# Kernel tuning notes

Measured on AMD Instinct MI355X. Metric: run time of the kernel, lower is better.

Reference implementation:

```python
import jax, jax.numpy as jnp
import numpy as np

MAX_ITER = 3  # module default init kwarg
B, S = 16, 128


def setup_inputs() -> dict:
    key = jax.random.key(0)
    k1, k2, k3 = jax.random.split(key, 3)
    s_span = jax.random.normal(k1, (B, S, S), dtype=jnp.float32)
    s_pair = jax.random.normal(k2, (B, S, S, S), dtype=jnp.float32)
    mask = jax.random.randint(k3, (B, S, S), 0, 2).astype(jnp.bool_)
    return {"s_span": s_span, "s_pair": s_pair, "mask": mask}


def reference(s_span, s_pair, mask):
    # Faithful batch-first translation of MFVIConstituency.mfvi + sigmoid.
    # torch code works in [S, S, B] layout; here we keep [B, S, S].
    seq_len = mask.shape[1]
    idx = jnp.arange(seq_len)
    # ls[i,j]=min(i,j), rs[i,j]=max(i,j) (stack(where(ones)).sort(0) trick)
    ls = jnp.minimum(idx[:, None], idx[None, :])  # [S, S]
    rs = jnp.maximum(idx[:, None], idx[None, :])  # [S, S]
    # exclude k == min(i,j) and k == max(i,j): [S, S, S] over (i, j, k)
    ne = (ls[:, :, None] != idx[None, None, :]) & (rs[:, :, None] != idx[None, None, :])
    # span_mask broadcast in torch aligns trailing dims -> indexed at (j, k):
    # mask2o[b,i,j,k] &= mask[b,k,j] | mask[b,j,k]
    span = mask | jnp.swapaxes(mask, 1, 2)  # [B, S, S] symmetric
    # mask2o[b,i,j,k] = mask[b,i,j] & ne[i,j,k] & span[b,j,k]
    mask2o = mask[:, :, :, None] & ne[None, :, :, :] & span[:, None, :, :]
    sp = s_pair * mask2o.astype(s_pair.dtype)  # [B, S, S, S]
    q = s_span
    for _ in range(MAX_ITER):
        q = jax.nn.sigmoid(q)
        # q_new[b,i,j] = s_span[b,i,j] + sum_k q[b,i,k] * sp[b,i,j,k]
        q = s_span + jnp.einsum('bik,bijk->bij', q, sp)
    return jax.nn.sigmoid(q)  # marginals [B, S, S]
```

## Files before the change

kernel.cpp:

```cpp
#include <hip/hip_runtime.h>
#include <hip/hip_bf16.h>


#define S 128
#define MB_STRIDE 132
#define PART_STRIDE 33

static __device__ __forceinline__ float fsig(float x) {
    return __builtin_amdgcn_rcpf(1.0f + __expf(-x));
}

__global__ __launch_bounds__(256, 2) void pack_masks(
    const int* __restrict__ mask, unsigned* __restrict__ spanw,
    unsigned* __restrict__ miw)
{
    __shared__ unsigned char mb[S * MB_STRIDE];
    const int t = threadIdx.x, b = blockIdx.x;
    const int* mrow = mask + (long long)b * (S * S);
    #pragma unroll
    for (int s2 = 0; s2 < 16; ++s2) {
        int f4 = t + 256 * s2;
        int j  = f4 >> 5;
        int k0 = (f4 & 31) * 4;
        int4 v = *(const int4*)(mrow + f4 * 4);
        unsigned packed = (v.x ? 1u : 0u)
                        | ((v.y ? 1u : 0u) << 8)
                        | ((v.z ? 1u : 0u) << 16)
                        | ((v.w ? 1u : 0u) << 24);
        *(unsigned*)(mb + j * MB_STRIDE + k0) = packed;
    }
    __syncthreads();
    #pragma unroll
    for (int r = 0; r < 2; ++r) {
        int task = t * 2 + r;
        int j = task >> 2, w = task & 3;
        unsigned sbits = 0, mbits = 0;
        #pragma unroll
        for (int c = 0; c < 32; ++c) {
            int k = w * 32 + c;
            unsigned mjk = mb[j * MB_STRIDE + k];
            unsigned mkj = mb[k * MB_STRIDE + j];
            sbits |= ((mjk | mkj) ? 1u : 0u) << c;
            mbits |= (mjk ? 1u : 0u) << c;
        }
        spanw[(b * S + j) * 4 + w] = sbits;
        miw  [(b * S + j) * 4 + w] = mbits;
    }
}

__global__ __launch_bounds__(256, 4) void mfvi_main(
    const float* __restrict__ s_span,
    const float* __restrict__ s_pair,
    const unsigned* __restrict__ spanw,
    const unsigned* __restrict__ miw,
    float* __restrict__ out)
{
    __shared__ float         part[S * PART_STRIDE];
    __shared__ unsigned      sw_l[S * 4];
    __shared__ float         prow[S];
    __shared__ float         qsv [S];
    __shared__ unsigned char act [S];
    __shared__ int           nact_s;

    const int t  = threadIdx.x;
    const int bi = blockIdx.x;
    const int i  = bi & (S - 1);
    const int b  = bi >> 7;
    const int row0 = t >> 5;
    const int c4   = (t & 31) * 4;
    const float* tile = s_pair + (long long)bi * (S * S);

    if (t < S) *(uint4*)&sw_l[t * 4] = *(const uint4*)&spanw[(b * S + t) * 4];
    if (t < S) {
        float sv = s_span[(long long)bi * S + t];
        qsv[t]  = sv;
        prow[t] = fsig(sv);
    }
    if (t < 64) {
        unsigned w0 = miw[(b * S + i) * 4 + (t >> 5)];
        bool a0 = (w0 >> (t & 31)) & 1u;
        unsigned long long b0 = __ballot(a0);
        int p0 = __popcll(b0 & ((1ull << t) - 1ull));
        if (a0) act[p0] = (unsigned char)t;
        int n0 = __popcll(b0);
        int j1 = t + 64;
        unsigned w1 = miw[(b * S + i) * 4 + (j1 >> 5)];
        bool a1 = (w1 >> (j1 & 31)) & 1u;
        unsigned long long b1 = __ballot(a1);
        int p1 = n0 + __popcll(b1 & ((1ull << t) - 1ull));
        if (a1) act[p1] = (unsigned char)j1;
        if (t == 0) nact_s = n0 + __popcll(b1);
    }
    __syncthreads();
    const int nact = nact_s;

    if (t < S) {
        bool mine = (miw[(b * S + i) * 4 + (t >> 5)] >> (t & 31)) & 1u;
        if (!mine) out[(long long)bi * S + t] = prow[t];
    }

    float4 v[16];
    #pragma unroll
    for (int s = 0; s < 16; ++s) {
        int idx = row0 + 8 * s;
        if (idx < nact) {
            int j = act[idx];
            v[s] = *(const float4*)(tile + j * S + c4);
        } else {
            v[s] = make_float4(0.f, 0.f, 0.f, 0.f);
        }
    }

    #pragma unroll
    for (int s = 0; s < 16; ++s) {
        int idx = row0 + 8 * s;
        if (idx < nact) {
            int j = act[idx];
            unsigned cw = sw_l[j * 4 + (c4 >> 5)];
            int lo = i < j ? i : j, hi = i < j ? j : i;
            if ((lo >> 5) == (c4 >> 5)) cw &= ~(1u << (lo & 31));
            if ((hi >> 5) == (c4 >> 5)) cw &= ~(1u << (hi & 31));
            unsigned cs = cw >> (c4 & 31);
            int m0 = ((int)(cs << 31)) >> 31;
            int m1 = ((int)(cs << 30)) >> 31;
            int m2 = ((int)(cs << 29)) >> 31;
            int m3 = ((int)(cs << 28)) >> 31;
            v[s].x = __int_as_float(__float_as_int(v[s].x) & m0);
            v[s].y = __int_as_float(__float_as_int(v[s].y) & m1);
            v[s].z = __int_as_float(__float_as_int(v[s].z) & m2);
            v[s].w = __int_as_float(__float_as_int(v[s].w) & m3);
        }
    }

    const int pcol = t & 31;
    #pragma unroll
    for (int it = 0; it < 3; ++it) {
        float4 p = *(const float4*)&prow[c4];
        #pragma unroll
        for (int s = 0; s < 16; ++s) {
            int idx = row0 + 8 * s;
            if (idx < nact) {
                float acc = v[s].x * p.x + v[s].y * p.y + v[s].z * p.z + v[s].w * p.w;
                part[idx * PART_STRIDE + pcol] = acc;
            }
        }
        __syncthreads();
        if (t < nact) {
            int j = act[t];
            float sum = 0.f;
            #pragma unroll
            for (int c = 0; c < 32; ++c) sum += part[t * PART_STRIDE + c];
            float q = qsv[j] + sum;
            if (it < 2) prow[j] = fsig(q);
            else        out[(long long)bi * S + j] = fsig(q);
        }
        if (it < 2) __syncthreads();
    }
}

extern "C" void kernel_launch(void* const* d_in, const int* in_sizes, int n_in,
                              void* d_out, int out_size, void* d_ws, size_t ws_size,
                              hipStream_t stream) {
    const float* s_span = (const float*)d_in[0];
    const float* s_pair = (const float*)d_in[1];
    const int*   mask   = (const int*)d_in[2];
    float*       out    = (float*)d_out;

    int num_rows = in_sizes[0] / S;
    int B        = in_sizes[2] / (S * S);

    unsigned* ws_span = (unsigned*)d_ws;
    unsigned* ws_mi   = ws_span + (size_t)B * S * 4;

    pack_masks<<<B, 256, 0, stream>>>(mask, ws_span, ws_mi);
    mfvi_main<<<num_rows, 256, 0, stream>>>(s_span, s_pair, ws_span, ws_mi, out);
}
```

Measured before the change: 191.2 us.

## Reduce row dot-products with wave shuffles and precompute active-row lists in pack kernel

The LDS partial-sum buffer and its extra barrier per iteration are replaced by an in-register butterfly reduction using xor shuffles across 32 lanes, and prow is double-buffered so only one barrier per iteration remains. Compaction of active rows moves from the main kernel into the mask-packing kernel, which writes per-row index lists and counts to workspace. Span masking is folded into the tile load loop, and unmasked outputs are written straight from the raw mask. The main kernel's startup gets simpler and LDS use drops, at the cost of more shuffle instructions, more predicated single-lane sigmoid work, and extra workspace traffic in the pack kernel.

```diff
diff --git a/kernel.cpp b/kernel.cpp
--- a/kernel.cpp
+++ b/kernel.cpp
@@ -4,15 +4,16 @@
 
 #define S 128
 #define MB_STRIDE 132
-#define PART_STRIDE 33
 
 static __device__ __forceinline__ float fsig(float x) {
     return __builtin_amdgcn_rcpf(1.0f + __expf(-x));
 }
 
 __global__ __launch_bounds__(256, 2) void pack_masks(
-    const int* __restrict__ mask, unsigned* __restrict__ spanw,
-    unsigned* __restrict__ miw)
+    const int* __restrict__ mask,
+    unsigned* __restrict__ spanw,
+    unsigned char* __restrict__ actg,
+    int* __restrict__ nactg)
 {
     __shared__ unsigned char mb[S * MB_STRIDE];
     const int t = threadIdx.x, b = blockIdx.x;
@@ -30,37 +31,50 @@
         *(unsigned*)(mb + j * MB_STRIDE + k0) = packed;
     }
     __syncthreads();
+
     #pragma unroll
     for (int r = 0; r < 2; ++r) {
         int task = t * 2 + r;
         int j = task >> 2, w = task & 3;
-        unsigned sbits = 0, mbits = 0;
+        unsigned sbits = 0;
         #pragma unroll
         for (int c = 0; c < 32; ++c) {
             int k = w * 32 + c;
-            unsigned mjk = mb[j * MB_STRIDE + k];
-            unsigned mkj = mb[k * MB_STRIDE + j];
-            sbits |= ((mjk | mkj) ? 1u : 0u) << c;
-            mbits |= (mjk ? 1u : 0u) << c;
+            sbits |= ((mb[j * MB_STRIDE + k] | mb[k * MB_STRIDE + j]) ? 1u : 0u) << c;
         }
         spanw[(b * S + j) * 4 + w] = sbits;
-        miw  [(b * S + j) * 4 + w] = mbits;
+    }
+
+    {
+        int wave = t >> 6, lane = t & 63;
+        for (int r = 0; r < 32; ++r) {
+            int i = wave * 32 + r;
+            unsigned char* dst = actg + (long long)(b * S + i) * S;
+            bool a0 = mb[i * MB_STRIDE + lane] != 0;
+            unsigned long long b0 = __ballot(a0);
+            int n0 = __popcll(b0);
+            if (a0) dst[__popcll(b0 & ((1ull << lane) - 1ull))] = (unsigned char)lane;
+            bool a1 = mb[i * MB_STRIDE + 64 + lane] != 0;
+            unsigned long long b1 = __ballot(a1);
+            if (a1) dst[n0 + __popcll(b1 & ((1ull << lane) - 1ull))] = (unsigned char)(64 + lane);
+            if (lane == 0) nactg[b * S + i] = n0 + __popcll(b1);
+        }
     }
 }
 
 __global__ __launch_bounds__(256, 4) void mfvi_main(
     const float* __restrict__ s_span,
     const float* __restrict__ s_pair,
+    const int* __restrict__ mask,
     const unsigned* __restrict__ spanw,
-    const unsigned* __restrict__ miw,
+    const unsigned char* __restrict__ actg,
+    const int* __restrict__ nactg,
     float* __restrict__ out)
 {
-    __shared__ float         part[S * PART_STRIDE];
     __shared__ unsigned      sw_l[S * 4];
-    __shared__ float         prow[S];
+    __shared__ float         prow2[2][S];
     __shared__ float         qsv [S];
-    __shared__ unsigned char act [S];
-    __shared__ int           nact_s;
+    __shared__ unsigned char act_l[S];
 
     const int t  = threadIdx.x;
     const int bi = blockIdx.x;
@@ -69,90 +83,75 @@
     const int row0 = t >> 5;
     const int c4   = (t & 31) * 4;
     const float* tile = s_pair + (long long)bi * (S * S);
+    const int nact = nactg[bi];
 
-    if (t < S) *(uint4*)&sw_l[t * 4] = *(const uint4*)&spanw[(b * S + t) * 4];
     if (t < S) {
+        act_l[t] = actg[(long long)bi * S + t];
+        *(uint4*)&sw_l[t * 4] = *(const uint4*)&spanw[(b * S + t) * 4];
         float sv = s_span[(long long)bi * S + t];
-        qsv[t]  = sv;
-        prow[t] = fsig(sv);
-    }
-    if (t < 64) {
-        unsigned w0 = miw[(b * S + i) * 4 + (t >> 5)];
-        bool a0 = (w0 >> (t & 31)) & 1u;
-        unsigned long long b0 = __ballot(a0);
-        int p0 = __popcll(b0 & ((1ull << t) - 1ull));
-        if (a0) act[p0] = (unsigned char)t;
-        int n0 = __popcll(b0);
-        int j1 = t + 64;
-        unsigned w1 = miw[(b * S + i) * 4 + (j1 >> 5)];
-        bool a1 = (w1 >> (j1 & 31)) & 1u;
-        unsigned long long b1 = __ballot(a1);
-        int p1 = n0 + __popcll(b1 & ((1ull << t) - 1ull));
-        if (a1) act[p1] = (unsigned char)j1;
-        if (t == 0) nact_s = n0 + __popcll(b1);
+        qsv[t] = sv;
+        float p0 = fsig(sv);
+        prow2[0][t] = p0;
+        prow2[1][t] = p0;
+        if (!mask[(long long)bi * S + t])
+            out[(long long)bi * S + t] = p0;
     }
     __syncthreads();
-    const int nact = nact_s;
-
-    if (t < S) {
-        bool mine = (miw[(b * S + i) * 4 + (t >> 5)] >> (t & 31)) & 1u;
-        if (!mine) out[(long long)bi * S + t] = prow[t];
-    }
 
     float4 v[16];
     #pragma unroll
     for (int s = 0; s < 16; ++s) {
         int idx = row0 + 8 * s;
         if (idx < nact) {
-            int j = act[idx];
-            v[s] = *(const float4*)(tile + j * S + c4);
+            int j = act_l[idx];
+            float4 x = *(const float4*)(tile + j * S + c4);
+            unsigned cw = sw_l[j * 4 + (c4 >> 5)];
+            int lo = i < j ? i : j, hi = i < j ? j : i;
+            if ((lo >> 5) == (c4 >> 5)) cw &= ~(1u << (lo & 31));
+            if ((hi >> 5) == (c4 >> 5)) cw &= ~(1u << (hi & 31));
+            unsigned cs = cw >> (c4 & 31);
+            x.x = __int_as_float(__float_as_int(x.x) & (((int)(cs << 31)) >> 31));
+            x.y = __int_as_float(__float_as_int(x.y) & (((int)(cs << 30)) >> 31));
+            x.z = __int_as_float(__float_as_int(x.z) & (((int)(cs << 29)) >> 31));
+            x.w = __int_as_float(__float_as_int(x.w) & (((int)(cs << 28)) >> 31));
+            v[s] = x;
         } else {
             v[s] = make_float4(0.f, 0.f, 0.f, 0.f);
         }
     }
 
     #pragma unroll
-    for (int s = 0; s < 16; ++s) {
-        int idx = row0 + 8 * s;
-        if (idx < nact) {
-            int j = act[idx];
-            unsigned cw = sw_l[j * 4 + (c4 >> 5)];
-            int lo = i < j ? i : j, hi = i < j ? j : i;
-            if ((lo >> 5) == (c4 >> 5)) cw &= ~(1u << (lo & 31));
-            if ((hi >> 5) == (c4 >> 5)) cw &= ~(1u << (hi & 31));
-            unsigned cs = cw >> (c4 & 31);
-            int m0 = ((int)(cs << 31)) >> 31;
-            int m1 = ((int)(cs << 30)) >> 31;
-            int m2 = ((int)(cs << 29)) >> 31;
-            int m3 = ((int)(cs << 28)) >> 31;
-            v[s].x = __int_as_float(__float_as_int(v[s].x) & m0);
-            v[s].y = __int_as_float(__float_as_int(v[s].y) & m1);
-            v[s].z = __int_as_float(__float_as_int(v[s].z) & m2);
-            v[s].w = __int_as_float(__float_as_int(v[s].w) & m3);
-        }
-    }
-
-    const int pcol = t & 31;
-    #pragma unroll
     for (int it = 0; it < 3; ++it) {
-        float4 p = *(const float4*)&prow[c4];
+        const float* pr = prow2[it & 1];
+        float*       pw = prow2[(it + 1) & 1];
+        float4 p = *(const float4*)&pr[c4];
+        float acc[16];
         #pragma unroll
         for (int s = 0; s < 16; ++s) {
             int idx = row0 + 8 * s;
-            if (idx < nact) {
-                float acc = v[s].x * p.x + v[s].y * p.y + v[s].z * p.z + v[s].w * p.w;
-                part[idx * PART_STRIDE + pcol] = acc;
+            acc[s] = (idx < nact)
+                   ? (v[s].x * p.x + v[s].y * p.y + v[s].z * p.z + v[s].w * p.w)
+                   : 0.f;
+        }
+        #pragma unroll
+        for (int s = 0; s < 16; ++s) {
+            acc[s] += __shfl_xor(acc[s], 1);
+            acc[s] += __shfl_xor(acc[s], 2);
+            acc[s] += __shfl_xor(acc[s], 4);
+            acc[s] += __shfl_xor(acc[s], 8);
+            acc[s] += __shfl_xor(acc[s], 16);
+        }
+        if ((t & 31) == 0) {
+            #pragma unroll
+            for (int s = 0; s < 16; ++s) {
+                int idx = row0 + 8 * s;
+                if (idx < nact) {
+                    int j = act_l[idx];
+                    float q = qsv[j] + acc[s];
+                    if (it < 2) pw[j] = fsig(q);
+                    else        out[(long long)bi * S + j] = fsig(q);
+                }
             }
-        }
-        __syncthreads();
-        if (t < nact) {
-            int j = act[t];
-            float sum = 0.f;
-            #pragma unroll
-            for (int c = 0; c < 32; ++c) sum += part[t * PART_STRIDE + c];
-            float q = qsv[j] + sum;
-            if (it < 2) prow[j] = fsig(q);
-            else        out[(long long)bi * S + j] = fsig(q);
         }
         if (it < 2) __syncthreads();
     }
@@ -169,9 +168,11 @@
     int num_rows = in_sizes[0] / S;
     int B        = in_sizes[2] / (S * S);
 
-    unsigned* ws_span = (unsigned*)d_ws;
-    unsigned* ws_mi   = ws_span + (size_t)B * S * 4;
+    unsigned*      ws_span = (unsigned*)d_ws;
+    unsigned char* ws_act  = (unsigned char*)(ws_span + (size_t)B * S * 4);
+    int*           ws_nact = (int*)(ws_act + (size_t)B * S * S);
 
-    pack_masks<<<B, 256, 0, stream>>>(mask, ws_span, ws_mi);
-    mfvi_main<<<num_rows, 256, 0, stream>>>(s_span, s_pair, ws_span, ws_mi, out);
+    pack_masks<<<B, 256, 0, stream>>>(mask, ws_span, ws_act, ws_nact);
+    mfvi_main<<<num_rows, 256, 0, stream>>>(s_span, s_pair, mask,
+                                            ws_span, ws_act, ws_nact, out);
 }
```

Result: slower. 212.9 us (+11.3%).
